# Kernel optimization log

Measured on AMD Instinct MI355X. Metric: run time of the kernel, lower is better.

The kernel has to match this reference:

```python
import jax, jax.numpy as jnp
import numpy as np

V, F, H, W, K, B, J = 50000, 100000, 256, 256, 1, 4, 256

def setup_inputs() -> dict:
    key = jax.random.key(0)
    ks = jax.random.split(key, 8)
    pix_to_face = jax.random.randint(ks[0], (1, H, W, K), 0, F, dtype=jnp.int32)
    bary = jax.random.uniform(ks[1], (1, H, W, K, 3), dtype=jnp.float32)
    bary = bary / jnp.sum(bary, axis=-1, keepdims=True)  # valid barycentric weights
    faces = jax.random.randint(ks[2], (F, 3), 0, V, dtype=jnp.int32)
    verts = jax.random.normal(ks[3], (V, 3), dtype=jnp.float32)
    vertex_normals = jax.random.normal(ks[4], (V, 3), dtype=jnp.float32)
    directions = jax.random.normal(ks[5], (B, J, 3), dtype=jnp.float32)
    directions = directions / jnp.linalg.norm(directions, axis=-1, keepdims=True)
    env_colors = jax.random.uniform(ks[6], (B, J, 3), dtype=jnp.float32)  # environment_map * sineweight
    texels = jax.random.uniform(ks[7], (1, H, W, 3), dtype=jnp.float32)
    return {"pix_to_face": pix_to_face, "bary_coords": bary, "faces": faces,
            "verts": verts, "vertex_normals": vertex_normals,
            "directions": directions, "env_colors": env_colors, "texels": texels}

def reference(pix_to_face, bary_coords, faces, verts, vertex_normals, directions, env_colors, texels):
    # interpolate_face_attributes: gather per-face vertex normals, bary-weighted sum
    faces_normals = vertex_normals[faces]                     # (F, 3verts, 3)
    attr = faces_normals[pix_to_face]                         # (1, H, W, K, 3verts, 3)
    pixel_normals = jnp.einsum('nhwkv,nhwkvc->nhwkc', bary_coords, attr)[:, :, :, 0, :]  # (1,H,W,3)
    # F.normalize(p=2, dim=-1, eps=1e-6): divide by clamped norm
    norm = jnp.maximum(jnp.linalg.norm(pixel_normals, axis=-1, keepdims=True), 1e-6)
    pixel_normals = pixel_normals / norm
    normals = jnp.broadcast_to(pixel_normals, (directions.shape[0],) + pixel_normals.shape[1:])  # (B,H,W,3)
    # diffuse dot products over all J lights, clamped to [0,1]
    diffuse = jnp.clip(jnp.einsum('bhwc,bjc->bhwj', normals, directions), 0.0, 1.0)  # (B,H,W,J)
    diffuse = jnp.einsum('bjc,bhwj->bhwc', env_colors, diffuse)                      # (B,H,W,3)
    colors = diffuse * texels
    return colors, diffuse, texels, normals
```

## Files before the change

### kernel.cpp

```cpp
#include <hip/hip_runtime.h>

#define NPIX  65536
#define BB    4
#define JJ    256


struct F3 { float x, y, z; };
struct I3 { int x, y, z; };

__global__ __launch_bounds__(256, 8) void shade_kernel(
    const int*   __restrict__ p2f,
    const float* __restrict__ bary,
    const int*   __restrict__ faces,
    const float* __restrict__ vnorm,
    const float* __restrict__ dirs,
    const float* __restrict__ env,
    const float* __restrict__ tex,
    float*       __restrict__ out)
{
    const int b     = blockIdx.x >> 9;
    const int pbase = (blockIdx.x & 511) << 7;
    const int t     = threadIdx.x;
    const int i     = t & 63;
    const int jq    = __builtin_amdgcn_readfirstlane(t >> 6);

    __shared__ float nlds[128][3];
    __shared__ float part[4][128][3];

    const F3* __restrict__ bary3  = (const F3*)bary;
    const I3* __restrict__ faces3 = (const I3*)faces;
    const F3* __restrict__ vn3    = (const F3*)vnorm;
    const F3* __restrict__ tex3   = (const F3*)tex;

    if (t < 128) {
        const int p = pbase + t;
        const int f = p2f[p];
        const I3 vv = faces3[f];
        const F3 bc = bary3[p];
        const F3 a0 = vn3[vv.x];
        const F3 a1 = vn3[vv.y];
        const F3 a2 = vn3[vv.z];
        float nx = bc.x*a0.x + bc.y*a1.x + bc.z*a2.x;
        float ny = bc.x*a0.y + bc.y*a1.y + bc.z*a2.y;
        float nz = bc.x*a0.z + bc.y*a1.z + bc.z*a2.z;
        const float inv = 1.0f / fmaxf(sqrtf(nx*nx + ny*ny + nz*nz), 1e-6f);
        nx *= inv; ny *= inv; nz *= inv;
        nlds[t][0] = nx; nlds[t][1] = ny; nlds[t][2] = nz;

        float* __restrict__ nor = out + (3*BB*NPIX*2 + 3*NPIX);
        const int o = 3*(b*NPIX + p);
        nor[o+0] = nx; nor[o+1] = ny; nor[o+2] = nz;

        if (b == 0) {
            const F3 tv = tex3[p];
            float* __restrict__ tx = out + 3*BB*NPIX*2;
            tx[3*p+0] = tv.x; tx[3*p+1] = tv.y; tx[3*p+2] = tv.z;
        }
    }
    __syncthreads();

    const float n0x = nlds[i][0],    n0y = nlds[i][1],    n0z = nlds[i][2];
    const float n1x = nlds[64+i][0], n1y = nlds[64+i][1], n1z = nlds[64+i][2];

    float a0r=0.f, a0g=0.f, a0b=0.f, a1r=0.f, a1g=0.f, a1b=0.f;
    const float* __restrict__ dp = dirs + b*(JJ*3) + jq*(64*3);
    const float* __restrict__ ep = env  + b*(JJ*3) + jq*(64*3);

    #pragma unroll 8
    for (int j = 0; j < 64; ++j) {
        const float dx = dp[3*j+0], dy = dp[3*j+1], dz = dp[3*j+2];
        const float er = ep[3*j+0], eg = ep[3*j+1], eb = ep[3*j+2];
        float w0 = fmaf(n0z, dz, fmaf(n0y, dy, n0x*dx));
        float w1 = fmaf(n1z, dz, fmaf(n1y, dy, n1x*dx));
        w0 = fminf(fmaxf(w0, 0.f), 1.f);
        w1 = fminf(fmaxf(w1, 0.f), 1.f);
        a0r = fmaf(er, w0, a0r); a0g = fmaf(eg, w0, a0g); a0b = fmaf(eb, w0, a0b);
        a1r = fmaf(er, w1, a1r); a1g = fmaf(eg, w1, a1g); a1b = fmaf(eb, w1, a1b);
    }

    const int w = t >> 6;
    part[w][i][0]    = a0r; part[w][i][1]    = a0g; part[w][i][2]    = a0b;
    part[w][64+i][0] = a1r; part[w][64+i][1] = a1g; part[w][64+i][2] = a1b;
    __syncthreads();

    if (t < 128) {
        const int p = pbase + t;
        const float sr = part[0][t][0]+part[1][t][0]+part[2][t][0]+part[3][t][0];
        const float sg = part[0][t][1]+part[1][t][1]+part[2][t][1]+part[3][t][1];
        const float sb = part[0][t][2]+part[1][t][2]+part[2][t][2]+part[3][t][2];

        const F3 tv = tex3[p];
        const int o = 3*(b*NPIX + p);
        out[o+0] = sr*tv.x; out[o+1] = sg*tv.y; out[o+2] = sb*tv.z;

        float* __restrict__ dif = out + 3*BB*NPIX;
        dif[o+0] = sr; dif[o+1] = sg; dif[o+2] = sb;
    }
}

extern "C" void kernel_launch(void* const* d_in, const int* in_sizes, int n_in,
                              void* d_out, int out_size, void* d_ws, size_t ws_size,
                              hipStream_t stream) {
    const int*   p2f   = (const int*)  d_in[0];
    const float* bary  = (const float*)d_in[1];
    const int*   faces = (const int*)  d_in[2];
    const float* vnorm = (const float*)d_in[4];
    const float* dirs  = (const float*)d_in[5];
    const float* env   = (const float*)d_in[6];
    const float* tex   = (const float*)d_in[7];
    float* out = (float*)d_out;

    const int grid = BB * (NPIX / 128);
    shade_kernel<<<grid, 256, 0, stream>>>(
        p2f, bary, faces, vnorm, dirs, env, tex, out);
}
```

Baseline: 19.72 us.

## Merge batch into 1024-thread blocks, pack math into float2, spread output stores across waves

Each block now handles all four batch entries for 128 pixels with 1024 threads, so the normal gather and normalisation run once per pixel rather than once per batch. The light loop uses two-wide vector FMAs to handle both pixel halves together, and the redundant clamp to 1 is dropped. The normal and texel output stores move to otherwise idle waves, and wave 0 of each batch does the final reduction. In exchange the grid has a quarter as many blocks, each much larger, which may reduce scheduling flexibility and occupancy.

```diff
diff --git a/kernel.cpp b/kernel.cpp
--- a/kernel.cpp
+++ b/kernel.cpp
@@ -8,7 +8,9 @@
 struct F3 { float x, y, z; };
 struct I3 { int x, y, z; };
 
-__global__ __launch_bounds__(256, 8) void shade_kernel(
+typedef float f2 __attribute__((ext_vector_type(2)));
+
+__global__ __launch_bounds__(1024, 8) void shade_kernel(
     const int*   __restrict__ p2f,
     const float* __restrict__ bary,
     const int*   __restrict__ faces,
@@ -18,14 +20,14 @@
     const float* __restrict__ tex,
     float*       __restrict__ out)
 {
-    const int b     = blockIdx.x >> 9;
-    const int pbase = (blockIdx.x & 511) << 7;
     const int t     = threadIdx.x;
-    const int i     = t & 63;
-    const int jq    = __builtin_amdgcn_readfirstlane(t >> 6);
+    const int L     = t & 63;
+    const int jq    = __builtin_amdgcn_readfirstlane((t >> 6) & 3);
+    const int b     = __builtin_amdgcn_readfirstlane(t >> 8);
+    const int pbase = blockIdx.x << 7;
 
-    __shared__ float nlds[128][3];
-    __shared__ float part[4][128][3];
+    __shared__ float4 nlds[128];
+    __shared__ f2     part[4][4][64][3];
 
     const F3* __restrict__ bary3  = (const F3*)bary;
     const I3* __restrict__ faces3 = (const I3*)faces;
@@ -45,24 +47,17 @@
         float nz = bc.x*a0.z + bc.y*a1.z + bc.z*a2.z;
         const float inv = 1.0f / fmaxf(sqrtf(nx*nx + ny*ny + nz*nz), 1e-6f);
         nx *= inv; ny *= inv; nz *= inv;
-        nlds[t][0] = nx; nlds[t][1] = ny; nlds[t][2] = nz;
-
-        float* __restrict__ nor = out + (3*BB*NPIX*2 + 3*NPIX);
-        const int o = 3*(b*NPIX + p);
-        nor[o+0] = nx; nor[o+1] = ny; nor[o+2] = nz;
-
-        if (b == 0) {
-            const F3 tv = tex3[p];
-            float* __restrict__ tx = out + 3*BB*NPIX*2;
-            tx[3*p+0] = tv.x; tx[3*p+1] = tv.y; tx[3*p+2] = tv.z;
-        }
+        nlds[t] = make_float4(nx, ny, nz, 0.f);
     }
     __syncthreads();
 
-    const float n0x = nlds[i][0],    n0y = nlds[i][1],    n0z = nlds[i][2];
-    const float n1x = nlds[64+i][0], n1y = nlds[64+i][1], n1z = nlds[64+i][2];
+    const float4 nA = nlds[L];
+    const float4 nB = nlds[64 + L];
+    const f2 nx = {nA.x, nB.x};
+    const f2 ny = {nA.y, nB.y};
+    const f2 nz = {nA.z, nB.z};
+    f2 ar = {0.f, 0.f}, ag = {0.f, 0.f}, ab = {0.f, 0.f};
 
-    float a0r=0.f, a0g=0.f, a0b=0.f, a1r=0.f, a1g=0.f, a1b=0.f;
     const float* __restrict__ dp = dirs + b*(JJ*3) + jq*(64*3);
     const float* __restrict__ ep = env  + b*(JJ*3) + jq*(64*3);
 
@@ -70,31 +65,53 @@
     for (int j = 0; j < 64; ++j) {
         const float dx = dp[3*j+0], dy = dp[3*j+1], dz = dp[3*j+2];
         const float er = ep[3*j+0], eg = ep[3*j+1], eb = ep[3*j+2];
-        float w0 = fmaf(n0z, dz, fmaf(n0y, dy, n0x*dx));
-        float w1 = fmaf(n1z, dz, fmaf(n1y, dy, n1x*dx));
-        w0 = fminf(fmaxf(w0, 0.f), 1.f);
-        w1 = fminf(fmaxf(w1, 0.f), 1.f);
-        a0r = fmaf(er, w0, a0r); a0g = fmaf(eg, w0, a0g); a0b = fmaf(eb, w0, a0b);
-        a1r = fmaf(er, w1, a1r); a1g = fmaf(eg, w1, a1g); a1b = fmaf(eb, w1, a1b);
+        f2 w = __builtin_elementwise_fma(nz, (f2){dz, dz},
+               __builtin_elementwise_fma(ny, (f2){dy, dy}, nx * (f2){dx, dx}));
+        w = __builtin_elementwise_max(w, (f2){0.f, 0.f});
+        ar = __builtin_elementwise_fma((f2){er, er}, w, ar);
+        ag = __builtin_elementwise_fma((f2){eg, eg}, w, ag);
+        ab = __builtin_elementwise_fma((f2){eb, eb}, w, ab);
     }
 
-    const int w = t >> 6;
-    part[w][i][0]    = a0r; part[w][i][1]    = a0g; part[w][i][2]    = a0b;
-    part[w][64+i][0] = a1r; part[w][64+i][1] = a1g; part[w][64+i][2] = a1b;
+    if (jq != 0) {
+        part[jq][b][L][0] = ar;
+        part[jq][b][L][1] = ag;
+        part[jq][b][L][2] = ab;
+    }
+    if (jq == 1) {
+        float* __restrict__ nor = out + (3*BB*NPIX*2 + 3*NPIX);
+        const int pA = pbase + L, pB = pbase + 64 + L;
+        const int oA = 3*(b*NPIX + pA), oB = 3*(b*NPIX + pB);
+        nor[oA+0] = nA.x; nor[oA+1] = nA.y; nor[oA+2] = nA.z;
+        nor[oB+0] = nB.x; nor[oB+1] = nB.y; nor[oB+2] = nB.z;
+    }
+    if (jq == 2 && b == 0) {
+        float* __restrict__ tx = out + 3*BB*NPIX*2;
+        const int pA = pbase + L, pB = pbase + 64 + L;
+        const F3 tA = tex3[pA], tB = tex3[pB];
+        tx[3*pA+0] = tA.x; tx[3*pA+1] = tA.y; tx[3*pA+2] = tA.z;
+        tx[3*pB+0] = tB.x; tx[3*pB+1] = tB.y; tx[3*pB+2] = tB.z;
+    }
     __syncthreads();
 
-    if (t < 128) {
-        const int p = pbase + t;
-        const float sr = part[0][t][0]+part[1][t][0]+part[2][t][0]+part[3][t][0];
-        const float sg = part[0][t][1]+part[1][t][1]+part[2][t][1]+part[3][t][1];
-        const float sb = part[0][t][2]+part[1][t][2]+part[2][t][2]+part[3][t][2];
+    if (jq == 0) {
+        f2 sr = ar, sg = ag, sb = ab;
+        #pragma unroll
+        for (int q = 1; q < 4; ++q) {
+            sr += part[q][b][L][0];
+            sg += part[q][b][L][1];
+            sb += part[q][b][L][2];
+        }
+        const int pA = pbase + L, pB = pbase + 64 + L;
+        const F3 tA = tex3[pA], tB = tex3[pB];
+        const int oA = 3*(b*NPIX + pA), oB = 3*(b*NPIX + pB);
 
-        const F3 tv = tex3[p];
-        const int o = 3*(b*NPIX + p);
-        out[o+0] = sr*tv.x; out[o+1] = sg*tv.y; out[o+2] = sb*tv.z;
+        out[oA+0] = sr.x*tA.x; out[oA+1] = sg.x*tA.y; out[oA+2] = sb.x*tA.z;
+        out[oB+0] = sr.y*tB.x; out[oB+1] = sg.y*tB.y; out[oB+2] = sb.y*tB.z;
 
         float* __restrict__ dif = out + 3*BB*NPIX;
-        dif[o+0] = sr; dif[o+1] = sg; dif[o+2] = sb;
+        dif[oA+0] = sr.x; dif[oA+1] = sg.x; dif[oA+2] = sb.x;
+        dif[oB+0] = sr.y; dif[oB+1] = sg.y; dif[oB+2] = sb.y;
     }
 }
 
@@ -110,7 +127,7 @@
     const float* tex   = (const float*)d_in[7];
     float* out = (float*)d_out;
 
-    const int grid = BB * (NPIX / 128);
-    shade_kernel<<<grid, 256, 0, stream>>>(
+    const int grid = NPIX / 128;
+    shade_kernel<<<grid, 1024, 0, stream>>>(
         p2f, bary, faces, vnorm, dirs, env, tex, out);
 }
```

After: 17.54 us. 11.1% less time.
